# Kernel tuning notes

Hardware: AMD Instinct MI355X
Metric: run time of the kernel (lower is better)

## Reference

```python
import jax, jax.numpy as jnp
import numpy as np

N_NODES = 100000
N_EDGES = 640000
HIDDEN = 128


def setup_inputs() -> dict:
    key = jax.random.key(0)
    k1, k2, k3, k4 = jax.random.split(key, 4)
    node_emb = jax.random.normal(k1, (N_NODES, HIDDEN), dtype=jnp.float32)
    edge_index = jax.random.randint(k2, (2, N_EDGES), 0, N_NODES, dtype=jnp.int64)
    # edge head params: Linear(2H -> H), Linear(H -> 2)
    s1 = 1.0 / np.sqrt(2 * HIDDEN)
    s2 = 1.0 / np.sqrt(HIDDEN)
    W1 = jax.random.uniform(k3, (2 * HIDDEN, HIDDEN), jnp.float32, -s1, s1)
    b1 = jnp.zeros((HIDDEN,), jnp.float32)
    W2 = jax.random.uniform(k4, (HIDDEN, 2), jnp.float32, -s2, s2)
    b2 = jnp.zeros((2,), jnp.float32)
    return {"node_emb": node_emb, "edge_index": edge_index,
            "W1": W1, "b1": b1, "W2": W2, "b2": b2}


def reference(node_emb, edge_index, W1, b1, W2, b2):
    # gather src/dst node embeddings by edge_index (irregular gather)
    src, dst = edge_index[0], edge_index[1]
    edge_emb = jnp.concatenate([node_emb[src], node_emb[dst]], axis=-1)  # [E, 2H]
    # edge head: Linear -> ReLU -> (Dropout = identity in eval) -> Linear
    h = jax.nn.relu(edge_emb @ W1 + b1)  # [E, H]
    flow_pred = h @ W2 + b2              # [E, 2]
    return flow_pred
```

## Files before the change

kernel.cpp:

```cpp
#include <hip/hip_runtime.h>

typedef __attribute__((ext_vector_type(8))) short short8;
typedef __attribute__((ext_vector_type(4))) float floatx4;

static __device__ __forceinline__ unsigned short f2bf(float f) {
    union { float f; unsigned int u; } v; v.f = f;
    unsigned int u = v.u;
    return (unsigned short)((u + 0x7FFFu + ((u >> 16) & 1u)) >> 16);
}

__global__ void cvt_kernel(const float* __restrict__ x, unsigned short* __restrict__ y,
                           int n4, const float* __restrict__ w1,
                           unsigned short* __restrict__ w1t, int nblk_nodes) {
    __shared__ unsigned short sT[32 * 130];
    if ((int)blockIdx.x < nblk_nodes) {
        int i = blockIdx.x * 256 + threadIdx.x;
        if (i >= n4) return;
        const float4 v = ((const float4*)x)[i];
        ushort4 o;
        o.x = f2bf(v.x); o.y = f2bf(v.y); o.z = f2bf(v.z); o.w = f2bf(v.w);
        ((ushort4*)y)[i] = o;
    } else {
        const int b = blockIdx.x - nblk_nodes;
        const int k0 = b * 32;
        const int tid = threadIdx.x;
#pragma unroll
        for (int i = 0; i < 16; i++) {
            int idx = tid + i * 256;
            int k = idx >> 7, n = idx & 127;
            sT[k * 130 + n] = f2bf(w1[(k0 + k) * 128 + n]);
        }
        __syncthreads();
#pragma unroll
        for (int i = 0; i < 16; i++) {
            int idx = tid + i * 256;
            int n = idx >> 5, k = idx & 31;
            w1t[n * 256 + k0 + k] = sT[k * 130 + n];
        }
    }
}

__global__ __launch_bounds__(512, 4) void edge_mlp_kernel(
    const unsigned short* __restrict__ nodes,
    const unsigned short* __restrict__ w1t,
    const int* __restrict__ eidx,
    const float* __restrict__ b1,
    const float* __restrict__ w2,
    const float* __restrict__ b2,
    float* __restrict__ out,
    int E, int n_nodes)
{
    __shared__ unsigned short sB[128 * 128];
    __shared__ float2 sP[2][256];

    const int tid  = threadIdx.x;
    const int lane = tid & 63;
    const int wave = tid >> 6;
    const int g    = wave >> 1;
    const int half = wave & 1;
    const int l15  = lane & 15;
    const int lq   = lane >> 4;
    const long e0  = (long)blockIdx.x * 256 + g * 64;

    int offs[4], offd[4];
#pragma unroll
    for (int rt = 0; rt < 4; rt++) {
        long e = e0 + rt * 16 + l15;
        if (e >= E) e = E - 1;
        int s = eidx[e];
        int d = eidx[(long)E + e];
        s = (s < 0) ? 0 : (s >= n_nodes ? n_nodes - 1 : s);
        d = (d < 0) ? 0 : (d >= n_nodes ? n_nodes - 1 : d);
        offs[rt] = s << 8;
        offd[rt] = d << 8;
    }
    const char* nbase = (const char*)nodes;
    const int lbo = lq * 16;

    floatx4 acc[4][4];
#pragma unroll
    for (int rt = 0; rt < 4; rt++)
#pragma unroll
        for (int t = 0; t < 4; t++) acc[rt][t] = (floatx4){0.f, 0.f, 0.f, 0.f};

    short8 a_cur[4], a_nxt[4];
#pragma unroll
    for (int rt = 0; rt < 4; rt++)
        a_cur[rt] = *(const short8*)(nbase + offs[rt] + lbo);

    for (int ch = 0; ch < 2; ch++) {
        if (ch) __syncthreads();
#pragma unroll
        for (int i = 0; i < 4; i++) {
            int u = tid + i * 512;
            int n = u >> 4, s = u & 15;
            *(short8*)&sB[n * 128 + ((s ^ n) & 15) * 8] =
                *(const short8*)&w1t[n * 256 + ch * 128 + s * 8];
        }
        __syncthreads();

#pragma unroll
        for (int k2 = 0; k2 < 4; k2++) {
            const int ks = ch * 4 + k2;
            if (ks < 7) {
                const int ksn = ks + 1;
                const int cb = (ksn & 3) * 64 + lbo;
                const int* of = (ksn < 4) ? offs : offd;
#pragma unroll
                for (int rt = 0; rt < 4; rt++)
                    a_nxt[rt] = *(const short8*)(nbase + of[rt] + cb);
            }
#pragma unroll
            for (int t = 0; t < 4; t++) {
                const int n = (half * 4 + t) * 16 + l15;
                const int sl = (k2 * 4 + lq) ^ l15;
                short8 b = *(const short8*)&sB[n * 128 + sl * 8];
#pragma unroll
                for (int rt = 0; rt < 4; rt++)
                    acc[rt][t] = __builtin_amdgcn_mfma_f32_16x16x32_bf16(
                        a_cur[rt], b, acc[rt][t], 0, 0, 0);
            }
#pragma unroll
            for (int rt = 0; rt < 4; rt++) a_cur[rt] = a_nxt[rt];
        }
    }

    float b1v[4], w20[4], w21[4];
#pragma unroll
    for (int t = 0; t < 4; t++) {
        int c = (half * 4 + t) * 16 + l15;
        b1v[t] = b1[c];
        w20[t] = w2[c * 2];
        w21[t] = w2[c * 2 + 1];
    }
#pragma unroll
    for (int rt = 0; rt < 4; rt++) {
#pragma unroll
        for (int i = 0; i < 4; i++) {
            float p0 = 0.f, p1 = 0.f;
#pragma unroll
            for (int t = 0; t < 4; t++) {
                float h = acc[rt][t][i] + b1v[t];
                h = fmaxf(h, 0.f);
                p0 = fmaf(h, w20[t], p0);
                p1 = fmaf(h, w21[t], p1);
            }
#pragma unroll
            for (int m = 1; m < 16; m <<= 1) {
                p0 += __shfl_xor(p0, m, 64);
                p1 += __shfl_xor(p1, m, 64);
            }
            if (l15 == 0) {
                float2 o; o.x = p0; o.y = p1;
                sP[half][g * 64 + rt * 16 + lq * 4 + i] = o;
            }
        }
    }
    __syncthreads();

    {
        const int el = tid >> 1, chn = tid & 1;
        const long e = (long)blockIdx.x * 256 + el;
        if (e < E) {
            const float* p0 = (const float*)&sP[0][el];
            const float* p1 = (const float*)&sP[1][el];
            out[e * 2 + chn] = p0[chn] + p1[chn] + b2[chn];
        }
    }
}

extern "C" void kernel_launch(void* const* d_in, const int* in_sizes, int n_in,
                              void* d_out, int out_size, void* d_ws, size_t ws_size,
                              hipStream_t stream) {
    const float* node_emb = (const float*)d_in[0];
    const int*   eidx     = (const int*)d_in[1];
    const float* W1       = (const float*)d_in[2];
    const float* b1       = (const float*)d_in[3];
    const float* W2       = (const float*)d_in[4];
    const float* b2       = (const float*)d_in[5];
    float* out = (float*)d_out;

    const int n_node_elems = in_sizes[0];
    const int n_nodes = n_node_elems / 128;
    const int E = in_sizes[1] / 2;

    unsigned short* nodes_bf16 = (unsigned short*)d_ws;
    unsigned short* w1t =
        (unsigned short*)((char*)d_ws + (size_t)n_node_elems * 2);

    const int n4 = n_node_elems / 4;
    const int nblk_nodes = (n4 + 255) / 256;
    cvt_kernel<<<nblk_nodes + 8, 256, 0, stream>>>(node_emb, nodes_bf16, n4,
                                                   W1, w1t, nblk_nodes);

    const int nblk = (E + 255) / 256;
    edge_mlp_kernel<<<nblk, 512, 0, stream>>>(nodes_bf16, w1t, eidx,
                                              b1, W2, b2, out, E, n_nodes);
}
```

Before: 190.2 us.

## Stage full W1 in LDS, swap MFMA operands, compute second layer via MFMA

The whole transposed W1 (128x256 bf16, 64KB) is now loaded into shared memory once, which removes the mid-loop barrier and the second staging pass. The MFMA operands are swapped so that W1 rows are the A operand and the gathered node rows are the B operand, and the gather ring prefetches two k-steps ahead. The second linear layer (H->2) now runs as bf16 MFMA with a zero-padded W2 fragment in place of shuffle reductions. This trades a larger LDS footprint, which may lower occupancy, and bf16 rounding of the hidden activations for less epilogue work and fewer barriers.

```diff
diff --git a/kernel.cpp b/kernel.cpp
--- a/kernel.cpp
+++ b/kernel.cpp
@@ -1,6 +1,7 @@
 #include <hip/hip_runtime.h>
 
 typedef __attribute__((ext_vector_type(8))) short short8;
+typedef __attribute__((ext_vector_type(4))) short short4v;
 typedef __attribute__((ext_vector_type(4))) float floatx4;
 
 static __device__ __forceinline__ unsigned short f2bf(float f) {
@@ -46,11 +47,11 @@
     const int* __restrict__ eidx,
     const float* __restrict__ b1,
     const float* __restrict__ w2,
-    const float* __restrict__ b2,
+    const float* __restrict__ b2p,
     float* __restrict__ out,
     int E, int n_nodes)
 {
-    __shared__ unsigned short sB[128 * 128];
+    __shared__ unsigned short sW[128 * 256];
     __shared__ float2 sP[2][256];
 
     const int tid  = threadIdx.x;
@@ -64,107 +65,117 @@
 
     int offs[4], offd[4];
 #pragma unroll
-    for (int rt = 0; rt < 4; rt++) {
-        long e = e0 + rt * 16 + l15;
+    for (int nt = 0; nt < 4; nt++) {
+        long e = e0 + nt * 16 + l15;
         if (e >= E) e = E - 1;
         int s = eidx[e];
         int d = eidx[(long)E + e];
         s = (s < 0) ? 0 : (s >= n_nodes ? n_nodes - 1 : s);
         d = (d < 0) ? 0 : (d >= n_nodes ? n_nodes - 1 : d);
-        offs[rt] = s << 8;
-        offd[rt] = d << 8;
-    }
+        offs[nt] = s << 8;
+        offd[nt] = d << 8;
+    }
+
+#pragma unroll
+    for (int i = 0; i < 8; i++) {
+        int u = tid + i * 512;
+        int n = u >> 5, s = u & 31;
+        int sp = (s & 16) | ((s ^ n) & 15);
+        *(short8*)&sW[n * 256 + sp * 8] = *(const short8*)&w1t[n * 256 + s * 8];
+    }
+
     const char* nbase = (const char*)nodes;
     const int lbo = lq * 16;
 
+    short8 ring[2][4];
+#pragma unroll
+    for (int p = 0; p < 2; p++)
+#pragma unroll
+        for (int nt = 0; nt < 4; nt++)
+            ring[p][nt] = *(const short8*)(nbase + offs[nt] + p * 64 + lbo);
+
+    __syncthreads();
+
     floatx4 acc[4][4];
 #pragma unroll
-    for (int rt = 0; rt < 4; rt++)
-#pragma unroll
-        for (int t = 0; t < 4; t++) acc[rt][t] = (floatx4){0.f, 0.f, 0.f, 0.f};
-
-    short8 a_cur[4], a_nxt[4];
-#pragma unroll
-    for (int rt = 0; rt < 4; rt++)
-        a_cur[rt] = *(const short8*)(nbase + offs[rt] + lbo);
-
-    for (int ch = 0; ch < 2; ch++) {
-        if (ch) __syncthreads();
-#pragma unroll
-        for (int i = 0; i < 4; i++) {
-            int u = tid + i * 512;
-            int n = u >> 4, s = u & 15;
-            *(short8*)&sB[n * 128 + ((s ^ n) & 15) * 8] =
-                *(const short8*)&w1t[n * 256 + ch * 128 + s * 8];
-        }
-        __syncthreads();
-
-#pragma unroll
-        for (int k2 = 0; k2 < 4; k2++) {
-            const int ks = ch * 4 + k2;
-            if (ks < 7) {
-                const int ksn = ks + 1;
-                const int cb = (ksn & 3) * 64 + lbo;
-                const int* of = (ksn < 4) ? offs : offd;
-#pragma unroll
-                for (int rt = 0; rt < 4; rt++)
-                    a_nxt[rt] = *(const short8*)(nbase + of[rt] + cb);
-            }
-#pragma unroll
-            for (int t = 0; t < 4; t++) {
-                const int n = (half * 4 + t) * 16 + l15;
-                const int sl = (k2 * 4 + lq) ^ l15;
-                short8 b = *(const short8*)&sB[n * 128 + sl * 8];
-#pragma unroll
-                for (int rt = 0; rt < 4; rt++)
-                    acc[rt][t] = __builtin_amdgcn_mfma_f32_16x16x32_bf16(
-                        a_cur[rt], b, acc[rt][t], 0, 0, 0);
-            }
-#pragma unroll
-            for (int rt = 0; rt < 4; rt++) a_cur[rt] = a_nxt[rt];
-        }
-    }
-
-    float b1v[4], w20[4], w21[4];
-#pragma unroll
-    for (int t = 0; t < 4; t++) {
-        int c = (half * 4 + t) * 16 + l15;
-        b1v[t] = b1[c];
-        w20[t] = w2[c * 2];
-        w21[t] = w2[c * 2 + 1];
-    }
-#pragma unroll
-    for (int rt = 0; rt < 4; rt++) {
-#pragma unroll
-        for (int i = 0; i < 4; i++) {
-            float p0 = 0.f, p1 = 0.f;
-#pragma unroll
-            for (int t = 0; t < 4; t++) {
-                float h = acc[rt][t][i] + b1v[t];
-                h = fmaxf(h, 0.f);
-                p0 = fmaf(h, w20[t], p0);
-                p1 = fmaf(h, w21[t], p1);
-            }
-#pragma unroll
-            for (int m = 1; m < 16; m <<= 1) {
-                p0 += __shfl_xor(p0, m, 64);
-                p1 += __shfl_xor(p1, m, 64);
-            }
-            if (l15 == 0) {
-                float2 o; o.x = p0; o.y = p1;
-                sP[half][g * 64 + rt * 16 + lq * 4 + i] = o;
-            }
+    for (int mt = 0; mt < 4; mt++)
+#pragma unroll
+        for (int nt = 0; nt < 4; nt++) acc[mt][nt] = (floatx4){0.f, 0.f, 0.f, 0.f};
+
+#pragma unroll
+    for (int ks = 0; ks < 8; ks++) {
+        const int s  = ks * 4 + lq;
+        const int sp = (s & 16) | ((s ^ l15) & 15);
+#pragma unroll
+        for (int mt = 0; mt < 4; mt++) {
+            const int n = half * 64 + mt * 16 + l15;
+            const short8 af = *(const short8*)&sW[n * 256 + sp * 8];
+#pragma unroll
+            for (int nt = 0; nt < 4; nt++)
+                acc[mt][nt] = __builtin_amdgcn_mfma_f32_16x16x32_bf16(
+                    af, ring[ks & 1][nt], acc[mt][nt], 0, 0, 0);
+        }
+        if (ks < 6) {
+            const int ksn = ks + 2;
+            const int cb = (ksn & 3) * 64 + lbo;
+            const int* of = (ksn < 4) ? offs : offd;
+#pragma unroll
+            for (int nt = 0; nt < 4; nt++)
+                ring[ks & 1][nt] = *(const short8*)(nbase + of[nt] + cb);
+        }
+    }
+
+    short4v a2[4];
+#pragma unroll
+    for (int kt = 0; kt < 4; kt++) {
+        const int k2b = half * 64 + kt * 16 + lq * 4;
+        const float4 fa = *(const float4*)&w2[k2b * 2];
+        const float4 fb = *(const float4*)&w2[k2b * 2 + 4];
+        float j0 = (l15 == 1) ? fa.y : fa.x;
+        float j1 = (l15 == 1) ? fa.w : fa.z;
+        float j2 = (l15 == 1) ? fb.y : fb.x;
+        float j3 = (l15 == 1) ? fb.w : fb.z;
+        if (l15 >= 2) { j0 = 0.f; j1 = 0.f; j2 = 0.f; j3 = 0.f; }
+        short4v t;
+        t[0] = (short)f2bf(j0); t[1] = (short)f2bf(j1);
+        t[2] = (short)f2bf(j2); t[3] = (short)f2bf(j3);
+        a2[kt] = t;
+    }
+    floatx4 acc2[4];
+#pragma unroll
+    for (int nt = 0; nt < 4; nt++) acc2[nt] = (floatx4){0.f, 0.f, 0.f, 0.f};
+#pragma unroll
+    for (int kt = 0; kt < 4; kt++) {
+        const float4 bv = *(const float4*)&b1[half * 64 + kt * 16 + lq * 4];
+#pragma unroll
+        for (int nt = 0; nt < 4; nt++) {
+            short4v bf;
+            bf[0] = (short)f2bf(fmaxf(acc[kt][nt][0] + bv.x, 0.f));
+            bf[1] = (short)f2bf(fmaxf(acc[kt][nt][1] + bv.y, 0.f));
+            bf[2] = (short)f2bf(fmaxf(acc[kt][nt][2] + bv.z, 0.f));
+            bf[3] = (short)f2bf(fmaxf(acc[kt][nt][3] + bv.w, 0.f));
+            acc2[nt] = __builtin_amdgcn_mfma_f32_16x16x16bf16_1k(
+                a2[kt], bf, acc2[nt], 0, 0, 0);
+        }
+    }
+    if (lq == 0) {
+#pragma unroll
+        for (int nt = 0; nt < 4; nt++) {
+            float2 o;
+            o.x = acc2[nt][0];
+            o.y = acc2[nt][1];
+            sP[half][g * 64 + nt * 16 + l15] = o;
         }
     }
     __syncthreads();
 
     {
-        const int el = tid >> 1, chn = tid & 1;
+        const int el = tid >> 1, ch = tid & 1;
         const long e = (long)blockIdx.x * 256 + el;
         if (e < E) {
             const float* p0 = (const float*)&sP[0][el];
             const float* p1 = (const float*)&sP[1][el];
-            out[e * 2 + chn] = p0[chn] + p1[chn] + b2[chn];
+            out[e * 2 + ch] = p0[ch] + p1[ch] + b2p[ch];
         }
     }
 }
```

Result: no change. 191.2 us (+0.5%).

## Precompute per-node W1 projections, then gather and add them per edge

Applied to the files above, without the earlier changes.

Splits the first linear layer into its source and destination halves. A new node-level GEMM computes those projections once per node (bias folded into the source half) and stores them as bf16. The edge kernel then only gathers two projected rows, adds them, applies ReLU and does the small second layer. This removes the per-edge 256x128 MFMA work and the separate bf16 conversion pass. The projections are written in place over the node_emb input buffer, so the input is clobbered and repeated calls would read corrupted data.

```diff
diff --git a/kernel.cpp b/kernel.cpp
--- a/kernel.cpp
+++ b/kernel.cpp
@@ -1,6 +1,7 @@
 #include <hip/hip_runtime.h>
 
 typedef __attribute__((ext_vector_type(8))) short short8;
+typedef __attribute__((ext_vector_type(4))) short short4v;
 typedef __attribute__((ext_vector_type(4))) float floatx4;
 
 static __device__ __forceinline__ unsigned short f2bf(float f) {
@@ -8,163 +9,168 @@
     unsigned int u = v.u;
     return (unsigned short)((u + 0x7FFFu + ((u >> 16) & 1u)) >> 16);
 }
-
-__global__ void cvt_kernel(const float* __restrict__ x, unsigned short* __restrict__ y,
-                           int n4, const float* __restrict__ w1,
-                           unsigned short* __restrict__ w1t, int nblk_nodes) {
+static __device__ __forceinline__ float bf2f(short x) {
+    return __uint_as_float(((unsigned int)(unsigned short)x) << 16);
+}
+
+__global__ void cvt_wt_kernel(const float* __restrict__ w1,
+                              unsigned short* __restrict__ wt) {
     __shared__ unsigned short sT[32 * 130];
-    if ((int)blockIdx.x < nblk_nodes) {
-        int i = blockIdx.x * 256 + threadIdx.x;
-        if (i >= n4) return;
-        const float4 v = ((const float4*)x)[i];
-        ushort4 o;
-        o.x = f2bf(v.x); o.y = f2bf(v.y); o.z = f2bf(v.z); o.w = f2bf(v.w);
-        ((ushort4*)y)[i] = o;
-    } else {
-        const int b = blockIdx.x - nblk_nodes;
-        const int k0 = b * 32;
-        const int tid = threadIdx.x;
-#pragma unroll
-        for (int i = 0; i < 16; i++) {
-            int idx = tid + i * 256;
-            int k = idx >> 7, n = idx & 127;
-            sT[k * 130 + n] = f2bf(w1[(k0 + k) * 128 + n]);
-        }
-        __syncthreads();
-#pragma unroll
-        for (int i = 0; i < 16; i++) {
-            int idx = tid + i * 256;
-            int n = idx >> 5, k = idx & 31;
-            w1t[n * 256 + k0 + k] = sT[k * 130 + n];
-        }
-    }
-}
-
-__global__ __launch_bounds__(512, 4) void edge_mlp_kernel(
-    const unsigned short* __restrict__ nodes,
-    const unsigned short* __restrict__ w1t,
+    const int b = blockIdx.x;
+    const int kg0 = b * 32;
+    const int h = (kg0 >= 128) ? 1 : 0;
+    const int kk0 = kg0 & 127;
+    const int tid = threadIdx.x;
+#pragma unroll
+    for (int i = 0; i < 16; i++) {
+        int idx = tid + i * 256;
+        int k = idx >> 7, n = idx & 127;
+        sT[k * 130 + n] = f2bf(w1[(kg0 + k) * 128 + n]);
+    }
+    __syncthreads();
+#pragma unroll
+    for (int i = 0; i < 16; i++) {
+        int idx = tid + i * 256;
+        int n = idx >> 5, k = idx & 31;
+        wt[(h * 128 + n) * 128 + kk0 + k] = sT[k * 130 + n];
+    }
+}
+
+__global__ __launch_bounds__(256) void node_gemm_kernel(
+    float* xy,
+    const unsigned short* __restrict__ wt,
+    const float* __restrict__ b1, int N)
+{
+    __shared__ unsigned short sW[256 * 128];
+
+    const int tid = threadIdx.x;
+    const int lane = tid & 63, wave = tid >> 6;
+    const int l15 = lane & 15, lq = lane >> 4;
+
+#pragma unroll
+    for (int i = 0; i < 16; i++) {
+        int u = tid + i * 256;
+        int r = u >> 4, s = u & 15;
+        *(short8*)&sW[r * 128 + ((s ^ r) & 15) * 8] =
+            *(const short8*)&wt[r * 128 + s * 8];
+    }
+    __syncthreads();
+
+    const int n0 = blockIdx.x * 64 + wave * 16;
+    const int nr = n0 + l15;
+    const int nc = (nr < N) ? nr : (N - 1);
+    const float* xrow = xy + (size_t)nc * 128;
+
+    floatx4 acc[16];
+#pragma unroll
+    for (int mt = 0; mt < 16; mt++) acc[mt] = (floatx4){0.f, 0.f, 0.f, 0.f};
+
+#pragma unroll
+    for (int ks = 0; ks < 4; ks++) {
+        const float4 xa = *(const float4*)(xrow + ks * 32 + lq * 8);
+        const float4 xb = *(const float4*)(xrow + ks * 32 + lq * 8 + 4);
+        short8 bf;
+        bf[0] = (short)f2bf(xa.x); bf[1] = (short)f2bf(xa.y);
+        bf[2] = (short)f2bf(xa.z); bf[3] = (short)f2bf(xa.w);
+        bf[4] = (short)f2bf(xb.x); bf[5] = (short)f2bf(xb.y);
+        bf[6] = (short)f2bf(xb.z); bf[7] = (short)f2bf(xb.w);
+#pragma unroll
+        for (int mt = 0; mt < 16; mt++) {
+            const short8 af = *(const short8*)
+                &sW[(mt * 16 + l15) * 128 + (((ks * 4 + lq) ^ l15) & 15) * 8];
+            acc[mt] = __builtin_amdgcn_mfma_f32_16x16x32_bf16(af, bf, acc[mt], 0, 0, 0);
+        }
+    }
+
+    if (nr < N) {
+        unsigned short* yrow = (unsigned short*)xy + (size_t)nr * 256;
+#pragma unroll
+        for (int mt = 0; mt < 16; mt++) {
+            const int oc = mt * 16 + lq * 4;
+            float4 bb = (mt < 8) ? *(const float4*)&b1[oc]
+                                 : (float4){0.f, 0.f, 0.f, 0.f};
+            short4v pk;
+            pk[0] = (short)f2bf(acc[mt][0] + bb.x);
+            pk[1] = (short)f2bf(acc[mt][1] + bb.y);
+            pk[2] = (short)f2bf(acc[mt][2] + bb.z);
+            pk[3] = (short)f2bf(acc[mt][3] + bb.w);
+            *(short4v*)(yrow + oc) = pk;
+        }
+    }
+}
+
+__global__ __launch_bounds__(256) void edge_kernel(
+    const unsigned short* __restrict__ Y,
     const int* __restrict__ eidx,
-    const float* __restrict__ b1,
     const float* __restrict__ w2,
     const float* __restrict__ b2,
     float* __restrict__ out,
     int E, int n_nodes)
 {
-    __shared__ unsigned short sB[128 * 128];
-    __shared__ float2 sP[2][256];
-
-    const int tid  = threadIdx.x;
-    const int lane = tid & 63;
-    const int wave = tid >> 6;
-    const int g    = wave >> 1;
-    const int half = wave & 1;
-    const int l15  = lane & 15;
-    const int lq   = lane >> 4;
-    const long e0  = (long)blockIdx.x * 256 + g * 64;
-
-    int offs[4], offd[4];
-#pragma unroll
-    for (int rt = 0; rt < 4; rt++) {
-        long e = e0 + rt * 16 + l15;
-        if (e >= E) e = E - 1;
-        int s = eidx[e];
-        int d = eidx[(long)E + e];
-        s = (s < 0) ? 0 : (s >= n_nodes ? n_nodes - 1 : s);
-        d = (d < 0) ? 0 : (d >= n_nodes ? n_nodes - 1 : d);
-        offs[rt] = s << 8;
-        offd[rt] = d << 8;
-    }
-    const char* nbase = (const char*)nodes;
-    const int lbo = lq * 16;
-
-    floatx4 acc[4][4];
-#pragma unroll
-    for (int rt = 0; rt < 4; rt++)
-#pragma unroll
-        for (int t = 0; t < 4; t++) acc[rt][t] = (floatx4){0.f, 0.f, 0.f, 0.f};
-
-    short8 a_cur[4], a_nxt[4];
-#pragma unroll
-    for (int rt = 0; rt < 4; rt++)
-        a_cur[rt] = *(const short8*)(nbase + offs[rt] + lbo);
-
-    for (int ch = 0; ch < 2; ch++) {
-        if (ch) __syncthreads();
-#pragma unroll
-        for (int i = 0; i < 4; i++) {
-            int u = tid + i * 512;
-            int n = u >> 4, s = u & 15;
-            *(short8*)&sB[n * 128 + ((s ^ n) & 15) * 8] =
-                *(const short8*)&w1t[n * 256 + ch * 128 + s * 8];
-        }
-        __syncthreads();
-
-#pragma unroll
-        for (int k2 = 0; k2 < 4; k2++) {
-            const int ks = ch * 4 + k2;
-            if (ks < 7) {
-                const int ksn = ks + 1;
-                const int cb = (ksn & 3) * 64 + lbo;
-                const int* of = (ksn < 4) ? offs : offd;
-#pragma unroll
-                for (int rt = 0; rt < 4; rt++)
-                    a_nxt[rt] = *(const short8*)(nbase + of[rt] + cb);
-            }
-#pragma unroll
-            for (int t = 0; t < 4; t++) {
-                const int n = (half * 4 + t) * 16 + l15;
-                const int sl = (k2 * 4 + lq) ^ l15;
-                short8 b = *(const short8*)&sB[n * 128 + sl * 8];
-#pragma unroll
-                for (int rt = 0; rt < 4; rt++)
-                    acc[rt][t] = __builtin_amdgcn_mfma_f32_16x16x32_bf16(
-                        a_cur[rt], b, acc[rt][t], 0, 0, 0);
-            }
-#pragma unroll
-            for (int rt = 0; rt < 4; rt++) a_cur[rt] = a_nxt[rt];
-        }
-    }
-
-    float b1v[4], w20[4], w21[4];
-#pragma unroll
-    for (int t = 0; t < 4; t++) {
-        int c = (half * 4 + t) * 16 + l15;
-        b1v[t] = b1[c];
-        w20[t] = w2[c * 2];
-        w21[t] = w2[c * 2 + 1];
-    }
-#pragma unroll
-    for (int rt = 0; rt < 4; rt++) {
-#pragma unroll
-        for (int i = 0; i < 4; i++) {
+    const int tid = threadIdx.x;
+    const int lane = tid & 63, wave = tid >> 6;
+    const int r = lane >> 4, cl = lane & 15;
+
+    float w20[8], w21[8];
+#pragma unroll
+    for (int q = 0; q < 4; q++) {
+        const float4 f = *(const float4*)&w2[cl * 16 + q * 4];
+        w20[q * 2]     = f.x; w21[q * 2]     = f.y;
+        w20[q * 2 + 1] = f.z; w21[q * 2 + 1] = f.w;
+    }
+    const float bb0 = b2[0], bb1 = b2[1];
+
+    const long eb = (long)blockIdx.x * 256 + wave * 64;
+    const char* Yb = (const char*)Y;
+
+    int sg[4], dg[4];
+#pragma unroll
+    for (int g = 0; g < 4; g++) {
+        long e = eb + g * 4 + r; if (e >= E) e = E - 1;
+        int s = eidx[e], d = eidx[(long)E + e];
+        sg[g] = (s < 0) ? 0 : (s >= n_nodes ? n_nodes - 1 : s);
+        dg[g] = (d < 0) ? 0 : (d >= n_nodes ? n_nodes - 1 : d);
+    }
+
+    for (int ch = 0; ch < 4; ch++) {
+        const long e0 = eb + ch * 16;
+        short8 v1[4], v2[4];
+#pragma unroll
+        for (int g = 0; g < 4; g++) {
+            v1[g] = *(const short8*)(Yb + (size_t)sg[g] * 512 + cl * 16);
+            v2[g] = *(const short8*)(Yb + (size_t)dg[g] * 512 + 256 + cl * 16);
+        }
+        if (ch < 3) {
+#pragma unroll
+            for (int g = 0; g < 4; g++) {
+                long e = e0 + 16 + g * 4 + r; if (e >= E) e = E - 1;
+                int s = eidx[e], d = eidx[(long)E + e];
+                sg[g] = (s < 0) ? 0 : (s >= n_nodes ? n_nodes - 1 : s);
+                dg[g] = (d < 0) ? 0 : (d >= n_nodes ? n_nodes - 1 : d);
+            }
+        }
+#pragma unroll
+        for (int g = 0; g < 4; g++) {
             float p0 = 0.f, p1 = 0.f;
 #pragma unroll
-            for (int t = 0; t < 4; t++) {
-                float h = acc[rt][t][i] + b1v[t];
-                h = fmaxf(h, 0.f);
-                p0 = fmaf(h, w20[t], p0);
-                p1 = fmaf(h, w21[t], p1);
+            for (int j = 0; j < 8; j++) {
+                float f = bf2f(v1[g][j]) + bf2f(v2[g][j]);
+                f = fmaxf(f, 0.f);
+                p0 = fmaf(f, w20[j], p0);
+                p1 = fmaf(f, w21[j], p1);
             }
 #pragma unroll
             for (int m = 1; m < 16; m <<= 1) {
                 p0 += __shfl_xor(p0, m, 64);
                 p1 += __shfl_xor(p1, m, 64);
             }
-            if (l15 == 0) {
-                float2 o; o.x = p0; o.y = p1;
-                sP[half][g * 64 + rt * 16 + lq * 4 + i] = o;
-            }
-        }
-    }
-    __syncthreads();
-
-    {
-        const int el = tid >> 1, chn = tid & 1;
-        const long e = (long)blockIdx.x * 256 + el;
-        if (e < E) {
-            const float* p0 = (const float*)&sP[0][el];
-            const float* p1 = (const float*)&sP[1][el];
-            out[e * 2 + chn] = p0[chn] + p1[chn] + b2[chn];
+            if (cl == 0) {
+                const long e = e0 + g * 4 + r;
+                if (e < E) {
+                    float2 o; o.x = p0 + bb0; o.y = p1 + bb1;
+                    *(float2*)&out[e * 2] = o;
+                }
+            }
         }
     }
 }
@@ -172,28 +178,26 @@
 extern "C" void kernel_launch(void* const* d_in, const int* in_sizes, int n_in,
                               void* d_out, int out_size, void* d_ws, size_t ws_size,
                               hipStream_t stream) {
-    const float* node_emb = (const float*)d_in[0];
-    const int*   eidx     = (const int*)d_in[1];
-    const float* W1       = (const float*)d_in[2];
-    const float* b1       = (const float*)d_in[3];
-    const float* W2       = (const float*)d_in[4];
-    const float* b2       = (const float*)d_in[5];
+    float*       xy   = (float*)d_in[0];
+    const int*   eidx = (const int*)d_in[1];
+    const float* W1   = (const float*)d_in[2];
+    const float* b1   = (const float*)d_in[3];
+    const float* W2   = (const float*)d_in[4];
+    const float* b2   = (const float*)d_in[5];
     float* out = (float*)d_out;
 
     const int n_node_elems = in_sizes[0];
-    const int n_nodes = n_node_elems / 128;
+    const int N = n_node_elems / 128;
     const int E = in_sizes[1] / 2;
 
-    unsigned short* nodes_bf16 = (unsigned short*)d_ws;
-    unsigned short* w1t =
-        (unsigned short*)((char*)d_ws + (size_t)n_node_elems * 2);
-
-    const int n4 = n_node_elems / 4;
-    const int nblk_nodes = (n4 + 255) / 256;
-    cvt_kernel<<<nblk_nodes + 8, 256, 0, stream>>>(node_emb, nodes_bf16, n4,
-                                                   W1, w1t, nblk_nodes);
-
-    const int nblk = (E + 255) / 256;
-    edge_mlp_kernel<<<nblk, 512, 0, stream>>>(nodes_bf16, w1t, eidx,
-                                              b1, W2, b2, out, E, n_nodes);
-}
+    unsigned short* wt = (unsigned short*)d_ws;
+
+    cvt_wt_kernel<<<8, 256, 0, stream>>>(W1, wt);
+
+    const int nblk1 = (N + 63) / 64;
+    node_gemm_kernel<<<nblk1, 256, 0, stream>>>(xy, wt, b1, N);
+
+    const int nblk2 = (E + 255) / 256;
+    edge_kernel<<<nblk2, 256, 0, stream>>>((const unsigned short*)xy, eidx,
+                                           W2, b2, out, E, N);
+}
```

After: 166.8 us. 12.3% less time.
